# Kernel optimization log

Measured on AMD Instinct MI355X. Metric: run time of the kernel, lower is better.

Reference implementation:

```python
import jax, jax.numpy as jnp
import numpy as np

VOCAB, EMB, SEQ_TOK, NHID, NLAYERS, NTOKEN = 400000, 300, 25, 256, 2, 2


def _lstm_layer(x, h0, c0, W_ih, W_hh, b_ih, b_hh):
    # x: [T, B, in], PyTorch gate order i, f, g, o
    def step(carry, xt):
        h, c = carry
        gates = xt @ W_ih.T + h @ W_hh.T + (b_ih + b_hh)
        i, f, g, o = jnp.split(gates, 4, axis=-1)
        c = jax.nn.sigmoid(f) * c + jax.nn.sigmoid(i) * jnp.tanh(g)
        h = jax.nn.sigmoid(o) * jnp.tanh(c)
        return (h, c), h
    (hT, cT), ys = jax.lax.scan(step, (h0, c0), x)
    return ys, hT, cT


def setup_inputs() -> dict:
    key = jax.random.key(0)
    ks = jax.random.split(key, 16)
    s = 0.05
    inp = {
        "input": jax.random.randint(ks[0], (1024, SEQ_TOK), 0, VOCAB),
        "h0": jnp.zeros((NLAYERS, 1024, NHID), jnp.float32),
        "c0": jnp.zeros((NLAYERS, 1024, NHID), jnp.float32),
        "emb_table": jax.random.normal(ks[1], (VOCAB, EMB), jnp.float32) * s,
        "fc_w": jax.random.normal(ks[2], (10, NHID), jnp.float32) * s,
        "fc_b": jnp.zeros((10,), jnp.float32),
        "dec_w": jax.random.normal(ks[3], (NTOKEN, 10), jnp.float32) * s,
        "dec_b": jnp.zeros((NTOKEN,), jnp.float32),
    }
    in_dims = [SEQ_TOK, NHID]
    for l in range(NLAYERS):
        inp[f"W_ih{l}"] = jax.random.normal(ks[4 + 4 * l], (4 * NHID, in_dims[l]), jnp.float32) * s
        inp[f"W_hh{l}"] = jax.random.normal(ks[5 + 4 * l], (4 * NHID, NHID), jnp.float32) * s
        inp[f"b_ih{l}"] = jnp.zeros((4 * NHID,), jnp.float32)
        inp[f"b_hh{l}"] = jnp.zeros((4 * NHID,), jnp.float32)
    return inp


def reference(input, h0, c0, emb_table, fc_w, fc_b, dec_w, dec_b,
              W_ih0, W_hh0, b_ih0, b_hh0, W_ih1, W_hh1, b_ih1, b_hh1):
    tokens = input.T                      # [25, B]
    B = tokens.shape[1]
    emb = emb_table[tokens]               # vectorized gather: [25, B, 300]
    emb = emb.reshape(300, B, 25)         # faithful to torch .view(300, B, 25)
    x = emb
    Ws = [(W_ih0, W_hh0, b_ih0, b_hh0), (W_ih1, W_hh1, b_ih1, b_hh1)]
    hs, cs = [], []
    for l in range(NLAYERS):
        x, hT, cT = _lstm_layer(x, h0[l], c0[l], *Ws[l])
        hs.append(hT); cs.append(cT)
    output = x                            # [300, B, nhid]
    hidden = (jnp.stack(hs), jnp.stack(cs))
    fc_out = jax.nn.relu(output @ fc_w.T + fc_b)  # [300, B, 10]
    decoded = fc_out[-1] @ dec_w.T + dec_b        # [B, ntoken]
    return (decoded.T, hidden[0], hidden[1])      # decoded.t(), (h, c)
```

## Files before the change

### kernel.cpp

```cpp
#include <hip/hip_runtime.h>
#include <stdint.h>

#define TSTEPS 300
#define BATCH  1024
#define MB     16
#define NWG    (BATCH / MB)
#define FRAGS_L0 36
#define FRAGS_L1 64
#define FRAGS_PW (FRAGS_L0 + FRAGS_L1)

typedef __bf16 bf16x8 __attribute__((ext_vector_type(8)));
typedef float  f32x4  __attribute__((ext_vector_type(4)));

__device__ __forceinline__ uint16_t f2bf(float f) {
  uint32_t u = __builtin_bit_cast(uint32_t, f);
  u += 0x7fffu + ((u >> 16) & 1u);
  return (uint16_t)(u >> 16);
}
__device__ __forceinline__ float bf2f(uint16_t h) {
  uint32_t u = ((uint32_t)h) << 16;
  return __builtin_bit_cast(float, u);
}
__device__ __forceinline__ float sigm(float x) { return 1.0f / (1.0f + __expf(-x)); }
__device__ __forceinline__ float tanh_(float x) {
  float e = __expf(2.0f * x);
  return (e - 1.0f) / (e + 1.0f);
}

__global__ void gather_x(const int* __restrict__ tok, const float* __restrict__ emb,
                         uint16_t* __restrict__ Xf) {
  int idx = blockIdx.x * 256 + threadIdx.x;
  int t    = idx >> 15;
  int rem  = idx & 32767;
  int wg   = rem >> 9;
  int e512 = rem & 511;
  int lane = e512 >> 3;
  int jj   = e512 & 7;
  int m = lane & 15, quad = lane >> 4;
  int k = quad * 8 + jj;
  float v = 0.0f;
  if (k < 25) {
    int b = wg * 16 + m;
    int n = (t * 1024 + b) * 25 + k;
    int s  = n / 307200;
    int r2 = n - s * 307200;
    int bb = r2 / 300;
    int e  = r2 - bb * 300;
    int token = tok[bb * 25 + s];
    v = emb[(size_t)token * 300 + e];
  }
  Xf[idx] = f2bf(v);
}

__global__ void pack_w(const float* __restrict__ Wih0, const float* __restrict__ Whh0,
                       const float* __restrict__ Wih1, const float* __restrict__ Whh1,
                       uint16_t* __restrict__ Wp) {
  int idx = blockIdx.x * 256 + threadIdx.x;
  int w   = idx / 51200;
  int rem = idx - w * 51200;
  int frag = rem >> 9;
  int e    = rem & 511;
  int lane = e >> 3, jj = e & 7;
  int nl = lane & 15, quad = lane >> 4;
  int kk = quad * 8 + jj;
  float v;
  if (frag < FRAGS_L0) {
    int ks = frag >> 2, nt = frag & 3;
    int n = nt * 256 + w * 16 + nl;
    if (ks == 0) v = (kk < 25) ? Wih0[n * 25 + kk] : 0.0f;
    else         v = Whh0[n * 256 + (ks - 1) * 32 + kk];
  } else {
    int f1 = frag - FRAGS_L0;
    int ks = f1 >> 2, nt = f1 & 3;
    int n = nt * 256 + w * 16 + nl;
    int k = ks * 32 + kk;
    v = (k < 256) ? Wih1[n * 256 + k] : Whh1[n * 256 + (k - 256)];
  }
  Wp[idx] = f2bf(v);
}

__global__ __launch_bounds__(1024, 4) void lstm_main(
    const float* __restrict__ h0in, const float* __restrict__ c0in,
    const float* __restrict__ fcw,  const float* __restrict__ fcb,
    const float* __restrict__ decw, const float* __restrict__ decb,
    const float* __restrict__ bih0, const float* __restrict__ bhh0,
    const float* __restrict__ bih1, const float* __restrict__ bhh1,
    const uint16_t* __restrict__ Xf, const uint16_t* __restrict__ Wp,
    float* __restrict__ out) {
  __shared__ uint16_t h0s[2][16][264];
  __shared__ uint16_t h1s[2][16][264];
  __shared__ float fcs[16][10];

  const int wg   = blockIdx.x;
  const int tid  = threadIdx.x;
  const int w    = tid >> 6;
  const int lane = tid & 63;
  const int jl   = lane & 15;
  const int quad = lane >> 4;
  const int jcol = w * 16 + jl;

  for (int idx = tid; idx < 16 * 256; idx += 1024) {
    int r = idx >> 8, k = idx & 255;
    int b = wg * 16 + r;
    h0s[0][r][k] = f2bf(h0in[(size_t)b * 256 + k]);
    h1s[0][r][k] = f2bf(h0in[262144 + (size_t)b * 256 + k]);
  }
  float c0r[4], c1r[4], h0v[4], h1v[4];
#pragma unroll
  for (int r = 0; r < 4; r++) {
    size_t b = wg * 16 + quad * 4 + r;
    c0r[r] = c0in[b * 256 + jcol];
    c1r[r] = c0in[262144 + b * 256 + jcol];
  }
  float bias0[4], bias1[4];
#pragma unroll
  for (int nt = 0; nt < 4; nt++) {
    int n = nt * 256 + jcol;
    bias0[nt] = bih0[n] + bhh0[n];
    bias1[nt] = bih1[n] + bhh1[n];
  }
  __syncthreads();

  const uint4* pw = (const uint4*)Wp + (size_t)(w * FRAGS_PW) * 64 + lane;
  const uint4* px = (const uint4*)Xf;

  bf16x8 bq[3][4];
#pragma unroll
  for (int s = 0; s < 3; s++)
#pragma unroll
    for (int nt = 0; nt < 4; nt++)
      bq[s][nt] = __builtin_bit_cast(bf16x8, pw[(s * 4 + nt) * 64]);
  bf16x8 xfrag = __builtin_bit_cast(bf16x8, px[(size_t)(0 * 64 + wg) * 64 + lane]);
  bf16x8 xnext;

  int p = 0;
  for (int tm = 0; tm < TSTEPS / 3; tm++) {
#pragma unroll
    for (int sub = 0; sub < 3; sub++) {
      const int t  = tm * 3 + sub;
      const int gb = sub * 25;

      f32x4 acc[4];
#pragma unroll
      for (int nt = 0; nt < 4; nt++)
        acc[nt] = (f32x4){bias0[nt], bias0[nt], bias0[nt], bias0[nt]};

      bf16x8 afrag = xfrag;
#pragma unroll
      for (int ks = 0; ks < 9; ks++) {
        const int slot = (gb + ks) % 3;
        bf16x8 anext = afrag;
        if (ks < 8)
          anext = __builtin_bit_cast(bf16x8,
                    *(const uint4*)&h0s[p][jl][ks * 32 + quad * 8]);
#pragma unroll
        for (int nt = 0; nt < 4; nt++)
          acc[nt] = __builtin_amdgcn_mfma_f32_16x16x32_bf16(afrag, bq[slot][nt], acc[nt], 0, 0, 0);
        {
          const int fo = ((gb + ks + 3) % 25) * 4;
#pragma unroll
          for (int nt = 0; nt < 4; nt++)
            bq[slot][nt] = __builtin_bit_cast(bf16x8, pw[(fo + nt) * 64]);
        }
        afrag = anext;
      }
#pragma unroll
      for (int r = 0; r < 4; r++) {
        float gi = sigm(acc[0][r]);
        float gf = sigm(acc[1][r]);
        float gg = tanh_(acc[2][r]);
        float go = sigm(acc[3][r]);
        float c = gf * c0r[r] + gi * gg;
        c0r[r] = c;
        float h = go * tanh_(c);
        h0v[r] = h;
        h0s[1 - p][quad * 4 + r][jcol] = f2bf(h);
      }
      __syncthreads();

#pragma unroll
      for (int nt = 0; nt < 4; nt++)
        acc[nt] = (f32x4){bias1[nt], bias1[nt], bias1[nt], bias1[nt]};

      afrag = __builtin_bit_cast(bf16x8, *(const uint4*)&h0s[1 - p][jl][quad * 8]);
#pragma unroll
      for (int ks = 0; ks < 16; ks++) {
        const int slot = (gb + 9 + ks) % 3;
        if (ks == 0) {
          int tn = (t + 1 < TSTEPS) ? t + 1 : 0;
          xnext = __builtin_bit_cast(bf16x8, px[(size_t)(tn * 64 + wg) * 64 + lane]);
        }
        bf16x8 anext = afrag;
        if (ks < 15) {
          const int ksn = ks + 1;
          const uint16_t* abase = (ksn < 8)
              ? &h0s[1 - p][jl][ksn * 32 + quad * 8]
              : &h1s[p][jl][(ksn - 8) * 32 + quad * 8];
          anext = __builtin_bit_cast(bf16x8, *(const uint4*)abase);
        }
#pragma unroll
        for (int nt = 0; nt < 4; nt++)
          acc[nt] = __builtin_amdgcn_mfma_f32_16x16x32_bf16(afrag, bq[slot][nt], acc[nt], 0, 0, 0);
        {
          const int fo = ((gb + 9 + ks + 3) % 25) * 4;
#pragma unroll
          for (int nt = 0; nt < 4; nt++)
            bq[slot][nt] = __builtin_bit_cast(bf16x8, pw[(fo + nt) * 64]);
        }
        afrag = anext;
      }
#pragma unroll
      for (int r = 0; r < 4; r++) {
        float gi = sigm(acc[0][r]);
        float gf = sigm(acc[1][r]);
        float gg = tanh_(acc[2][r]);
        float go = sigm(acc[3][r]);
        float c = gf * c1r[r] + gi * gg;
        c1r[r] = c;
        float h = go * tanh_(c);
        h1v[r] = h;
        h1s[1 - p][quad * 4 + r][jcol] = f2bf(h);
      }
      __syncthreads();
      p ^= 1;
      xfrag = xnext;
    }
  }

  float* outH = out + 2048;
  float* outC = out + 2048 + 524288;
#pragma unroll
  for (int r = 0; r < 4; r++) {
    size_t b = wg * 16 + quad * 4 + r;
    outH[b * 256 + jcol]          = h0v[r];
    outH[262144 + b * 256 + jcol] = h1v[r];
    outC[b * 256 + jcol]          = c0r[r];
    outC[262144 + b * 256 + jcol] = c1r[r];
  }
  if (tid < 160) {
    int r = tid / 10, ju = tid - r * 10;
    float s = fcb[ju];
    for (int k = 0; k < 256; k++)
      s += bf2f(h1s[p][r][k]) * fcw[ju * 256 + k];
    fcs[r][ju] = fmaxf(s, 0.0f);
  }
  __syncthreads();
  if (tid < 32) {
    int r = tid & 15, m = tid >> 4;
    float d = decb[m];
#pragma unroll
    for (int q = 0; q < 10; q++) d += fcs[r][q] * decw[m * 10 + q];
    out[(size_t)m * 1024 + wg * 16 + r] = d;
  }
}

extern "C" void kernel_launch(void* const* d_in, const int* in_sizes, int n_in,
                              void* d_out, int out_size, void* d_ws, size_t ws_size,
                              hipStream_t stream) {
  const int*   tok  = (const int*)d_in[0];
  const float* h0   = (const float*)d_in[1];
  const float* c0   = (const float*)d_in[2];
  const float* emb  = (const float*)d_in[3];
  const float* fcw  = (const float*)d_in[4];
  const float* fcb  = (const float*)d_in[5];
  const float* decw = (const float*)d_in[6];
  const float* decb = (const float*)d_in[7];
  const float* Wih0 = (const float*)d_in[8];
  const float* Whh0 = (const float*)d_in[9];
  const float* bih0 = (const float*)d_in[10];
  const float* bhh0 = (const float*)d_in[11];
  const float* Wih1 = (const float*)d_in[12];
  const float* Whh1 = (const float*)d_in[13];
  const float* bih1 = (const float*)d_in[14];
  const float* bhh1 = (const float*)d_in[15];

  uint16_t* Xf  = (uint16_t*)d_ws;
  uint16_t* Wpk = Xf + 9830400;

  gather_x<<<38400, 256, 0, stream>>>(tok, emb, Xf);
  pack_w<<<3200, 256, 0, stream>>>(Wih0, Whh0, Wih1, Whh1, Wpk);
  lstm_main<<<NWG, 1024, 0, stream>>>(h0, c0, fcw, fcb, decw, decb,
                                      bih0, bhh0, bih1, bhh1, Xf, Wpk,
                                      (float*)d_out);
}
```

Baseline: 14.06 ms.

## Keep all LSTM weight fragments resident in registers across timesteps

Loads all 100 weight fragments per wave into registers once, before the time loop, instead of streaming them from global memory through a 3-slot ring buffer on every step. This removes repeated global/L2 weight traffic on the recurrent critical path and simplifies the loop to a single timestep body. The cost is about 400 VGPRs per lane for weights alone, which risks spills or lower occupancy; final h/c stores move inside the loop under a last-step guard.

```diff
diff --git a/kernel.cpp b/kernel.cpp
--- a/kernel.cpp
+++ b/kernel.cpp
@@ -105,7 +105,7 @@
     h0s[0][r][k] = f2bf(h0in[(size_t)b * 256 + k]);
     h1s[0][r][k] = f2bf(h0in[262144 + (size_t)b * 256 + k]);
   }
-  float c0r[4], c1r[4], h0v[4], h1v[4];
+  float c0r[4], c1r[4];
 #pragma unroll
   for (int r = 0; r < 4; r++) {
     size_t b = wg * 16 + quad * 4 + r;
@@ -119,124 +119,104 @@
     bias0[nt] = bih0[n] + bhh0[n];
     bias1[nt] = bih1[n] + bhh1[n];
   }
-  __syncthreads();
 
   const uint4* pw = (const uint4*)Wp + (size_t)(w * FRAGS_PW) * 64 + lane;
+  bf16x8 wreg[FRAGS_PW];
+#pragma unroll
+  for (int f = 0; f < FRAGS_PW; f++)
+    wreg[f] = __builtin_bit_cast(bf16x8, pw[f * 64]);
+
   const uint4* px = (const uint4*)Xf;
-
-  bf16x8 bq[3][4];
-#pragma unroll
-  for (int s = 0; s < 3; s++)
-#pragma unroll
-    for (int nt = 0; nt < 4; nt++)
-      bq[s][nt] = __builtin_bit_cast(bf16x8, pw[(s * 4 + nt) * 64]);
   bf16x8 xfrag = __builtin_bit_cast(bf16x8, px[(size_t)(0 * 64 + wg) * 64 + lane]);
   bf16x8 xnext;
 
-  int p = 0;
-  for (int tm = 0; tm < TSTEPS / 3; tm++) {
-#pragma unroll
-    for (int sub = 0; sub < 3; sub++) {
-      const int t  = tm * 3 + sub;
-      const int gb = sub * 25;
-
-      f32x4 acc[4];
-#pragma unroll
-      for (int nt = 0; nt < 4; nt++)
-        acc[nt] = (f32x4){bias0[nt], bias0[nt], bias0[nt], bias0[nt]};
-
-      bf16x8 afrag = xfrag;
-#pragma unroll
-      for (int ks = 0; ks < 9; ks++) {
-        const int slot = (gb + ks) % 3;
-        bf16x8 anext = afrag;
-        if (ks < 8)
-          anext = __builtin_bit_cast(bf16x8,
-                    *(const uint4*)&h0s[p][jl][ks * 32 + quad * 8]);
-#pragma unroll
-        for (int nt = 0; nt < 4; nt++)
-          acc[nt] = __builtin_amdgcn_mfma_f32_16x16x32_bf16(afrag, bq[slot][nt], acc[nt], 0, 0, 0);
-        {
-          const int fo = ((gb + ks + 3) % 25) * 4;
-#pragma unroll
-          for (int nt = 0; nt < 4; nt++)
-            bq[slot][nt] = __builtin_bit_cast(bf16x8, pw[(fo + nt) * 64]);
-        }
-        afrag = anext;
-      }
-#pragma unroll
-      for (int r = 0; r < 4; r++) {
-        float gi = sigm(acc[0][r]);
-        float gf = sigm(acc[1][r]);
-        float gg = tanh_(acc[2][r]);
-        float go = sigm(acc[3][r]);
-        float c = gf * c0r[r] + gi * gg;
-        c0r[r] = c;
-        float h = go * tanh_(c);
-        h0v[r] = h;
-        h0s[1 - p][quad * 4 + r][jcol] = f2bf(h);
-      }
-      __syncthreads();
-
-#pragma unroll
-      for (int nt = 0; nt < 4; nt++)
-        acc[nt] = (f32x4){bias1[nt], bias1[nt], bias1[nt], bias1[nt]};
-
-      afrag = __builtin_bit_cast(bf16x8, *(const uint4*)&h0s[1 - p][jl][quad * 8]);
-#pragma unroll
-      for (int ks = 0; ks < 16; ks++) {
-        const int slot = (gb + 9 + ks) % 3;
-        if (ks == 0) {
-          int tn = (t + 1 < TSTEPS) ? t + 1 : 0;
-          xnext = __builtin_bit_cast(bf16x8, px[(size_t)(tn * 64 + wg) * 64 + lane]);
-        }
-        bf16x8 anext = afrag;
-        if (ks < 15) {
-          const int ksn = ks + 1;
-          const uint16_t* abase = (ksn < 8)
-              ? &h0s[1 - p][jl][ksn * 32 + quad * 8]
-              : &h1s[p][jl][(ksn - 8) * 32 + quad * 8];
-          anext = __builtin_bit_cast(bf16x8, *(const uint4*)abase);
-        }
-#pragma unroll
-        for (int nt = 0; nt < 4; nt++)
-          acc[nt] = __builtin_amdgcn_mfma_f32_16x16x32_bf16(afrag, bq[slot][nt], acc[nt], 0, 0, 0);
-        {
-          const int fo = ((gb + 9 + ks + 3) % 25) * 4;
-#pragma unroll
-          for (int nt = 0; nt < 4; nt++)
-            bq[slot][nt] = __builtin_bit_cast(bf16x8, pw[(fo + nt) * 64]);
-        }
-        afrag = anext;
-      }
-#pragma unroll
-      for (int r = 0; r < 4; r++) {
-        float gi = sigm(acc[0][r]);
-        float gf = sigm(acc[1][r]);
-        float gg = tanh_(acc[2][r]);
-        float go = sigm(acc[3][r]);
-        float c = gf * c1r[r] + gi * gg;
-        c1r[r] = c;
-        float h = go * tanh_(c);
-        h1v[r] = h;
-        h1s[1 - p][quad * 4 + r][jcol] = f2bf(h);
-      }
-      __syncthreads();
-      p ^= 1;
-      xfrag = xnext;
-    }
-  }
-
   float* outH = out + 2048;
   float* outC = out + 2048 + 524288;
-#pragma unroll
-  for (int r = 0; r < 4; r++) {
-    size_t b = wg * 16 + quad * 4 + r;
-    outH[b * 256 + jcol]          = h0v[r];
-    outH[262144 + b * 256 + jcol] = h1v[r];
-    outC[b * 256 + jcol]          = c0r[r];
-    outC[262144 + b * 256 + jcol] = c1r[r];
-  }
+
+  __syncthreads();
+
+  int p = 0;
+  for (int t = 0; t < TSTEPS; t++) {
+    f32x4 acc[4];
+#pragma unroll
+    for (int nt = 0; nt < 4; nt++)
+      acc[nt] = (f32x4){bias0[nt], bias0[nt], bias0[nt], bias0[nt]};
+
+    bf16x8 afrag = xfrag;
+#pragma unroll
+    for (int ks = 0; ks < 9; ks++) {
+      bf16x8 anext = afrag;
+      if (ks < 8)
+        anext = __builtin_bit_cast(bf16x8,
+                  *(const uint4*)&h0s[p][jl][ks * 32 + quad * 8]);
+#pragma unroll
+      for (int nt = 0; nt < 4; nt++)
+        acc[nt] = __builtin_amdgcn_mfma_f32_16x16x32_bf16(afrag, wreg[ks * 4 + nt], acc[nt], 0, 0, 0);
+      afrag = anext;
+    }
+#pragma unroll
+    for (int r = 0; r < 4; r++) {
+      float gi = sigm(acc[0][r]);
+      float gf = sigm(acc[1][r]);
+      float gg = tanh_(acc[2][r]);
+      float go = sigm(acc[3][r]);
+      float c = gf * c0r[r] + gi * gg;
+      c0r[r] = c;
+      float h = go * tanh_(c);
+      h0s[1 - p][quad * 4 + r][jcol] = f2bf(h);
+      if (t == TSTEPS - 1) {
+        size_t b = wg * 16 + quad * 4 + r;
+        outH[b * 256 + jcol] = h;
+        outC[b * 256 + jcol] = c;
+      }
+    }
+    __syncthreads();
+
+#pragma unroll
+    for (int nt = 0; nt < 4; nt++)
+      acc[nt] = (f32x4){bias1[nt], bias1[nt], bias1[nt], bias1[nt]};
+
+    afrag = __builtin_bit_cast(bf16x8, *(const uint4*)&h0s[1 - p][jl][quad * 8]);
+#pragma unroll
+    for (int ks = 0; ks < 16; ks++) {
+      if (ks == 0) {
+        int tn = (t + 1 < TSTEPS) ? t + 1 : 0;
+        xnext = __builtin_bit_cast(bf16x8, px[(size_t)(tn * 64 + wg) * 64 + lane]);
+      }
+      bf16x8 anext = afrag;
+      if (ks < 15) {
+        const int ksn = ks + 1;
+        const uint16_t* abase = (ksn < 8)
+            ? &h0s[1 - p][jl][ksn * 32 + quad * 8]
+            : &h1s[p][jl][(ksn - 8) * 32 + quad * 8];
+        anext = __builtin_bit_cast(bf16x8, *(const uint4*)abase);
+      }
+#pragma unroll
+      for (int nt = 0; nt < 4; nt++)
+        acc[nt] = __builtin_amdgcn_mfma_f32_16x16x32_bf16(afrag, wreg[FRAGS_L0 + ks * 4 + nt], acc[nt], 0, 0, 0);
+      afrag = anext;
+    }
+#pragma unroll
+    for (int r = 0; r < 4; r++) {
+      float gi = sigm(acc[0][r]);
+      float gf = sigm(acc[1][r]);
+      float gg = tanh_(acc[2][r]);
+      float go = sigm(acc[3][r]);
+      float c = gf * c1r[r] + gi * gg;
+      c1r[r] = c;
+      float h = go * tanh_(c);
+      h1s[1 - p][quad * 4 + r][jcol] = f2bf(h);
+      if (t == TSTEPS - 1) {
+        size_t b = wg * 16 + quad * 4 + r;
+        outH[262144 + b * 256 + jcol] = h;
+        outC[262144 + b * 256 + jcol] = c;
+      }
+    }
+    __syncthreads();
+    p ^= 1;
+    xfrag = xnext;
+  }
+
   if (tid < 160) {
     int r = tid / 10, ju = tid - r * 10;
     float s = fcb[ju];
```

After: 13.36 ms. 5.0% less time.
